# Kernel tuning notes

Measured on AMD Instinct MI355X. Metric: run time of the kernel, lower is better.

The kernel has to match this reference:

```python
import jax, jax.numpy as jnp
import numpy as np

B, T, IN = 65536, 28, 28
H_ENC, H_DEC, N_CLS = 4, 28, 10


def _lstm_params(key, in_dim, hidden):
    k1, k2, k3 = jax.random.split(key, 3)
    s = 1.0 / np.sqrt(hidden)
    Wih = jax.random.uniform(k1, (4 * hidden, in_dim), jnp.float32, -s, s)
    Whh = jax.random.uniform(k2, (4 * hidden, hidden), jnp.float32, -s, s)
    b = jax.random.uniform(k3, (4 * hidden,), jnp.float32, -s, s)  # b_ih + b_hh fused
    return Wih, Whh, b


def setup_inputs() -> dict:
    key = jax.random.key(0)
    kx, ke, kd, ku1, ku2 = jax.random.split(key, 5)
    enc_Wih, enc_Whh, enc_b = _lstm_params(ke, IN, H_ENC)
    dec_Wih, dec_Whh, dec_b = _lstm_params(kd, H_ENC, H_DEC)
    s = 1.0 / np.sqrt(H_DEC)
    U_W = jax.random.uniform(ku1, (N_CLS, H_DEC), jnp.float32, -s, s)
    U_b = jax.random.uniform(ku2, (N_CLS,), jnp.float32, -s, s)
    return {
        "x": jax.random.normal(kx, (B, T, IN), dtype=jnp.float32),
        "enc_Wih": enc_Wih, "enc_Whh": enc_Whh, "enc_b": enc_b,
        "dec_Wih": dec_Wih, "dec_Whh": dec_Whh, "dec_b": dec_b,
        "U_W": U_W, "U_b": U_b,
    }


def _lstm(x, Wih, Whh, b):
    """batch_first LSTM, zero init state. PyTorch gate order i,f,g,o."""
    Bn = x.shape[0]
    H = Whh.shape[1]
    # precompute input projection for all timesteps: [B,T,4H]
    xw = jnp.einsum('bti,gi->btg', x, Wih) + b
    h0 = jnp.zeros((Bn, H), x.dtype)

    def step(carry, xt):
        h, c = carry
        gates = xt + h @ Whh.T
        i, f, g, o = jnp.split(gates, 4, axis=-1)
        c = jax.nn.sigmoid(f) * c + jax.nn.sigmoid(i) * jnp.tanh(g)
        h = jax.nn.sigmoid(o) * jnp.tanh(c)
        return (h, c), h

    (h, c), hs = jax.lax.scan(step, (h0, h0), jnp.swapaxes(xw, 0, 1))
    return jnp.swapaxes(hs, 0, 1), h, c  # [B,T,H], [B,H], [B,H]


def reference(x, enc_Wih, enc_Whh, enc_b, dec_Wih, dec_Whh, dec_b, U_W, U_b):
    x = x.reshape(B, T, IN)
    z, _, _ = _lstm(x, enc_Wih, enc_Whh, enc_b)          # [B,T,4]
    out, h, _ = _lstm(z, dec_Wih, dec_Whh, dec_b)        # [B,T,28], h:[B,28]
    logits = h[None] @ U_W.T + U_b                        # [1,B,10] (h has num_layers=1 leading dim)
    prediction = jax.nn.softmax(logits, axis=2)
    return out, prediction
```

## Files before the change

### kernel.cpp

```cpp
#include <hip/hip_runtime.h>

#define B_TOTAL 65536
#define T_STEPS 28

typedef float f2 __attribute__((ext_vector_type(2)));

__device__ __forceinline__ float frcp(float x) { return __builtin_amdgcn_rcpf(x); }
__device__ __forceinline__ float sigf(float x) { return frcp(1.0f + __expf(-x)); }
__device__ __forceinline__ float tanhf_(float x) { return 2.0f * frcp(1.0f + __expf(-2.0f * x)) - 1.0f; }

__global__ void repack_kernel(const float* __restrict__ eWih, const float* __restrict__ eWhh,
                              const float* __restrict__ eb,
                              const float* __restrict__ dWih, const float* __restrict__ dWhh,
                              const float* __restrict__ db,
                              const float* __restrict__ UW, const float* __restrict__ Ub,
                              float* __restrict__ w)
{
    const int p = threadIdx.x;
    for (int idx = p; idx < 4 * 132; idx += 256) {
        int k = idx / 132, r = idx % 132;
        float v;
        if (r < 4) v = eb[r * 4 + k];
        else {
            int g = (r - 4) / 32, j = (r - 4) % 32;
            v = (j < 28) ? eWih[(g * 4 + k) * 28 + j] : eWhh[(g * 4 + k) * 4 + (j - 28)];
        }
        w[k * 132 + r] = v;
    }
    for (int idx = p; idx < 28 * 132; idx += 256) {
        int k = idx / 132, r = idx % 132;
        float v;
        if (r < 4) v = db[r * 28 + k];
        else {
            int g = (r - 4) / 32, j = (r - 4) % 32;
            v = (j < 28) ? dWhh[(g * 28 + k) * 28 + j] : dWih[(g * 28 + k) * 4 + (j - 28)];
        }
        w[528 + k * 132 + r] = v;
    }
    for (int idx = p; idx < 10 * 32; idx += 256) {
        int c = idx / 32, r = idx % 32;
        float v = (r == 0) ? Ub[c] : ((r <= 28) ? UW[c * 28 + (r - 1)] : 0.f);
        w[4224 + c * 32 + r] = v;
    }
}

#define XB   0
#define HD0  7680
#define HD1  15360
#define HE   23040

__global__ __launch_bounds__(256, 4)
void lstm_main(const float* __restrict__ x, const float* __restrict__ w,
               float* __restrict__ out, float* __restrict__ pred)
{
    __shared__ char lb[25088];

    const int tid  = threadIdx.x;
    const int lane = tid & 63;
    const int s    = __builtin_amdgcn_readfirstlane(tid >> 6);
    const int e0   = blockIdx.x * 64;

    int goff[7], stb[7];
#pragma unroll
    for (int q = 0; q < 7; q++) {
        int idx = tid + 256 * q;
        int i = idx / 28;
        int k = idx - 28 * i;
        goff[q] = i * 784 + k;
        stb[q]  = i * 120 + k * 4;
    }

    const float* __restrict__ xblk = x + (size_t)e0 * 784;
    float* __restrict__ oblk       = out + (size_t)e0 * 784;

#pragma unroll
    for (int q = 0; q < 7; q++)
        *(float*)(lb + XB + stb[q]) = xblk[goff[q]];
    for (int i2 = tid; i2 < 1920; i2 += 256) ((float*)(lb + HD0))[i2] = 0.f;
    ((float*)(lb + HE))[tid] = 0.f;
    __syncthreads();

    const float* __restrict__ wenc = w + s * 132;
    const char* xrow = lb + XB + lane * 120;

    float ce = 0.f;
    float cd[7];
#pragma unroll
    for (int r = 0; r < 7; r++) cd[r] = 0.f;

    int hdc = HD0, hdn = HD1;

    for (int t = 0; t < T_STEPS; ++t) {
        const int p = t & 1;

        float xr[7];
        if (t < T_STEPS - 1) {
#pragma unroll
            for (int q = 0; q < 7; q++)
                xr[q] = xblk[goff[q] + (t + 1) * 28];
        }

        {
            const f2* xp2 = (const f2*)xrow;
            const f2 hep0 = *(const f2*)(lb + HE + p * 1024 + lane * 16);
            const f2 hep1 = *(const f2*)(lb + HE + p * 1024 + lane * 16 + 8);
            const f2* wg0 = (const f2*)(wenc + 4);
            const f2* wg1 = (const f2*)(wenc + 36);
            const f2* wg2 = (const f2*)(wenc + 68);
            const f2* wg3 = (const f2*)(wenc + 100);
            f2 a0 = {wenc[0], 0.f}, a1 = {wenc[1], 0.f};
            f2 a2 = {wenc[2], 0.f}, a3 = {wenc[3], 0.f};
#pragma unroll
            for (int j = 0; j < 14; j++) {
                const f2 v = xp2[j];
                a0 = __builtin_elementwise_fma(wg0[j], v, a0);
                a1 = __builtin_elementwise_fma(wg1[j], v, a1);
                a2 = __builtin_elementwise_fma(wg2[j], v, a2);
                a3 = __builtin_elementwise_fma(wg3[j], v, a3);
            }
            a0 = __builtin_elementwise_fma(wg0[14], hep0, a0);
            a1 = __builtin_elementwise_fma(wg1[14], hep0, a1);
            a2 = __builtin_elementwise_fma(wg2[14], hep0, a2);
            a3 = __builtin_elementwise_fma(wg3[14], hep0, a3);
            a0 = __builtin_elementwise_fma(wg0[15], hep1, a0);
            a1 = __builtin_elementwise_fma(wg1[15], hep1, a1);
            a2 = __builtin_elementwise_fma(wg2[15], hep1, a2);
            a3 = __builtin_elementwise_fma(wg3[15], hep1, a3);
            const float gi = a0.x + a0.y, gf = a1.x + a1.y;
            const float gg = a2.x + a2.y, go = a3.x + a3.y;
            ce = sigf(gf) * ce + sigf(gi) * tanhf_(gg);
            *(float*)(lb + HE + (p ^ 1) * 1024 + lane * 16 + s * 4) =
                sigf(go) * tanhf_(ce);
        }
        __syncthreads();

        {
            const f2 hz0 = *(const f2*)(lb + HE + (p ^ 1) * 1024 + lane * 16);
            const f2 hz1 = *(const f2*)(lb + HE + (p ^ 1) * 1024 + lane * 16 + 8);
            const char* hcr = lb + hdc + lane * 120;
            char* hwr = lb + hdn + lane * 120 + s * 28;
#pragma unroll
            for (int r = 0; r < 7; r++) {
                asm volatile("" ::: "memory");
                const float* __restrict__ wrow = w + 528 + (s * 7 + r) * 132;
                const f2* wg0 = (const f2*)(wrow + 4);
                const f2* wg1 = (const f2*)(wrow + 36);
                const f2* wg2 = (const f2*)(wrow + 68);
                const f2* wg3 = (const f2*)(wrow + 100);
                const f2* hc2 = (const f2*)hcr;
                f2 a0 = {wrow[0], 0.f}, a1 = {wrow[1], 0.f};
                f2 a2 = {wrow[2], 0.f}, a3 = {wrow[3], 0.f};
#pragma unroll
                for (int j = 0; j < 14; j++) {
                    const f2 v = hc2[j];
                    a0 = __builtin_elementwise_fma(wg0[j], v, a0);
                    a1 = __builtin_elementwise_fma(wg1[j], v, a1);
                    a2 = __builtin_elementwise_fma(wg2[j], v, a2);
                    a3 = __builtin_elementwise_fma(wg3[j], v, a3);
                }
                a0 = __builtin_elementwise_fma(wg0[14], hz0, a0);
                a1 = __builtin_elementwise_fma(wg1[14], hz0, a1);
                a2 = __builtin_elementwise_fma(wg2[14], hz0, a2);
                a3 = __builtin_elementwise_fma(wg3[14], hz0, a3);
                a0 = __builtin_elementwise_fma(wg0[15], hz1, a0);
                a1 = __builtin_elementwise_fma(wg1[15], hz1, a1);
                a2 = __builtin_elementwise_fma(wg2[15], hz1, a2);
                a3 = __builtin_elementwise_fma(wg3[15], hz1, a3);
                const float gi = a0.x + a0.y, gf = a1.x + a1.y;
                const float gg = a2.x + a2.y, go = a3.x + a3.y;
                const float cc = sigf(gf) * cd[r] + sigf(gi) * tanhf_(gg);
                cd[r] = cc;
                *(float*)(hwr + r * 4) = sigf(go) * tanhf_(cc);
            }
        }

        if (t < T_STEPS - 1) {
#pragma unroll
            for (int q = 0; q < 7; q++)
                *(float*)(lb + XB + stb[q]) = xr[q];
        }
        __syncthreads();

        {
            const char* hsrc = lb + hdn;
#pragma unroll
            for (int q = 0; q < 7; q++)
                oblk[goff[q] + t * 28] = *(const float*)(hsrc + stb[q]);
        }
        const int tmp = hdc; hdc = hdn; hdn = tmp;
    }

    if (s == 0) {
        float hf[28];
        const f2* hc2 = (const f2*)(lb + hdc + lane * 120);
#pragma unroll
        for (int j = 0; j < 14; j++) {
            const f2 hp = hc2[j];
            hf[2 * j] = hp.x; hf[2 * j + 1] = hp.y;
        }
        float lg[10];
#pragma unroll
        for (int c = 0; c < 10; c++) {
            const float* __restrict__ ur = w + 4224 + c * 32;
            float a = ur[0];
#pragma unroll
            for (int j = 0; j < 28; j++) a = fmaf(ur[1 + j], hf[j], a);
            lg[c] = a;
        }
        float m = lg[0];
#pragma unroll
        for (int c = 1; c < 10; c++) m = fmaxf(m, lg[c]);
        float sum = 0.f;
#pragma unroll
        for (int c = 0; c < 10; c++) { lg[c] = __expf(lg[c] - m); sum += lg[c]; }
        const float inv = frcp(sum);
        float* __restrict__ pr = pred + (size_t)(e0 + lane) * 10;
#pragma unroll
        for (int c = 0; c < 10; c++) pr[c] = lg[c] * inv;
    }
}

extern "C" void kernel_launch(void* const* d_in, const int* in_sizes, int n_in,
                              void* d_out, int out_size, void* d_ws, size_t ws_size,
                              hipStream_t stream) {
    const float* x    = (const float*)d_in[0];
    const float* eWih = (const float*)d_in[1];
    const float* eWhh = (const float*)d_in[2];
    const float* eb   = (const float*)d_in[3];
    const float* dWih = (const float*)d_in[4];
    const float* dWhh = (const float*)d_in[5];
    const float* db   = (const float*)d_in[6];
    const float* UW   = (const float*)d_in[7];
    const float* Ub   = (const float*)d_in[8];

    float* w    = (float*)d_ws;
    float* out  = (float*)d_out;
    float* pred = out + (size_t)B_TOTAL * T_STEPS * 28;

    repack_kernel<<<dim3(1), dim3(256), 0, stream>>>(eWih, eWhh, eb, dWih, dWhh, db, UW, Ub, w);
    lstm_main<<<dim3(B_TOTAL / 64), dim3(256), 0, stream>>>(x, w, out, pred);
}
```

Measured before the change: 542.0 us.

## Software-pipeline encoder one step ahead to halve barriers per timestep

Restructures the time loop so the encoder step for t+1 runs in the same phase as the decoder step for t, with double-buffered x, encoder-h and decoder-h LDS regions. This cuts the block barriers per timestep from two to one, and the barrier becomes a lightweight lgkmcnt wait plus s_barrier. The x prefetch now runs two steps ahead, and output stores are delayed by one step. In exchange LDS grows from about 25KB to 32KB per block, which may limit occupancy.

```diff
diff --git a/kernel.cpp b/kernel.cpp
--- a/kernel.cpp
+++ b/kernel.cpp
@@ -8,6 +8,10 @@
 __device__ __forceinline__ float frcp(float x) { return __builtin_amdgcn_rcpf(x); }
 __device__ __forceinline__ float sigf(float x) { return frcp(1.0f + __expf(-x)); }
 __device__ __forceinline__ float tanhf_(float x) { return 2.0f * frcp(1.0f + __expf(-2.0f * x)) - 1.0f; }
+
+__device__ __forceinline__ void bar_lds() {
+    asm volatile("s_waitcnt lgkmcnt(0)\n\ts_barrier" ::: "memory");
+}
 
 __global__ void repack_kernel(const float* __restrict__ eWih, const float* __restrict__ eWhh,
                               const float* __restrict__ eb,
@@ -44,16 +48,18 @@
     }
 }
 
-#define XB   0
-#define HD0  7680
-#define HD1  15360
-#define HE   23040
+#define XA   0
+#define XB1  7680
+#define HDA  15360
+#define HDB  23040
+#define HEA  30720
+#define HEB  31744
 
 __global__ __launch_bounds__(256, 4)
 void lstm_main(const float* __restrict__ x, const float* __restrict__ w,
                float* __restrict__ out, float* __restrict__ pred)
 {
-    __shared__ char lb[25088];
+    __shared__ char lb[32768];
 
     const int tid  = threadIdx.x;
     const int lane = tid & 63;
@@ -73,72 +79,74 @@
     const float* __restrict__ xblk = x + (size_t)e0 * 784;
     float* __restrict__ oblk       = out + (size_t)e0 * 784;
 
-#pragma unroll
-    for (int q = 0; q < 7; q++)
-        *(float*)(lb + XB + stb[q]) = xblk[goff[q]];
-    for (int i2 = tid; i2 < 1920; i2 += 256) ((float*)(lb + HD0))[i2] = 0.f;
-    ((float*)(lb + HE))[tid] = 0.f;
-    __syncthreads();
-
     const float* __restrict__ wenc = w + s * 132;
-    const char* xrow = lb + XB + lane * 120;
 
     float ce = 0.f;
     float cd[7];
 #pragma unroll
     for (int r = 0; r < 7; r++) cd[r] = 0.f;
 
-    int hdc = HD0, hdn = HD1;
+    auto enc_step = [&](const int xbase, const int hrd, const int hwr) {
+        const f2* xp2 = (const f2*)(lb + xbase + lane * 120);
+        const f2 hep0 = *(const f2*)(lb + hrd + lane * 16);
+        const f2 hep1 = *(const f2*)(lb + hrd + lane * 16 + 8);
+        const f2* wg0 = (const f2*)(wenc + 4);
+        const f2* wg1 = (const f2*)(wenc + 36);
+        const f2* wg2 = (const f2*)(wenc + 68);
+        const f2* wg3 = (const f2*)(wenc + 100);
+        f2 a0 = {wenc[0], 0.f}, a1 = {wenc[1], 0.f};
+        f2 a2 = {wenc[2], 0.f}, a3 = {wenc[3], 0.f};
+#pragma unroll
+        for (int j = 0; j < 14; j++) {
+            const f2 v = xp2[j];
+            a0 = __builtin_elementwise_fma(wg0[j], v, a0);
+            a1 = __builtin_elementwise_fma(wg1[j], v, a1);
+            a2 = __builtin_elementwise_fma(wg2[j], v, a2);
+            a3 = __builtin_elementwise_fma(wg3[j], v, a3);
+        }
+        a0 = __builtin_elementwise_fma(wg0[14], hep0, a0);
+        a1 = __builtin_elementwise_fma(wg1[14], hep0, a1);
+        a2 = __builtin_elementwise_fma(wg2[14], hep0, a2);
+        a3 = __builtin_elementwise_fma(wg3[14], hep0, a3);
+        a0 = __builtin_elementwise_fma(wg0[15], hep1, a0);
+        a1 = __builtin_elementwise_fma(wg1[15], hep1, a1);
+        a2 = __builtin_elementwise_fma(wg2[15], hep1, a2);
+        a3 = __builtin_elementwise_fma(wg3[15], hep1, a3);
+        const float gi = a0.x + a0.y, gf = a1.x + a1.y;
+        const float gg = a2.x + a2.y, go = a3.x + a3.y;
+        ce = sigf(gf) * ce + sigf(gi) * tanhf_(gg);
+        *(float*)(lb + hwr + lane * 16 + s * 4) = sigf(go) * tanhf_(ce);
+    };
+
+#pragma unroll
+    for (int q = 0; q < 7; q++) {
+        *(float*)(lb + XA  + stb[q]) = xblk[goff[q]];
+        *(float*)(lb + XB1 + stb[q]) = xblk[goff[q] + 28];
+    }
+    for (int i2 = tid; i2 < 1920; i2 += 256) ((float*)(lb + HDB))[i2] = 0.f;
+    ((float*)(lb + HEB))[tid] = 0.f;
+    bar_lds();
+
+    enc_step(XA, HEB, HEA);
+    bar_lds();
+
+    int hdc = HDB, hdn = HDA;
+    int her = HEA, hew = HEB;
+    int xe  = XB1, xw  = XA;
 
     for (int t = 0; t < T_STEPS; ++t) {
-        const int p = t & 1;
-
         float xr[7];
-        if (t < T_STEPS - 1) {
+        if (t < T_STEPS - 2) {
 #pragma unroll
             for (int q = 0; q < 7; q++)
-                xr[q] = xblk[goff[q] + (t + 1) * 28];
+                xr[q] = xblk[goff[q] + (t + 2) * 28];
         }
 
         {
-            const f2* xp2 = (const f2*)xrow;
-            const f2 hep0 = *(const f2*)(lb + HE + p * 1024 + lane * 16);
-            const f2 hep1 = *(const f2*)(lb + HE + p * 1024 + lane * 16 + 8);
-            const f2* wg0 = (const f2*)(wenc + 4);
-            const f2* wg1 = (const f2*)(wenc + 36);
-            const f2* wg2 = (const f2*)(wenc + 68);
-            const f2* wg3 = (const f2*)(wenc + 100);
-            f2 a0 = {wenc[0], 0.f}, a1 = {wenc[1], 0.f};
-            f2 a2 = {wenc[2], 0.f}, a3 = {wenc[3], 0.f};
-#pragma unroll
-            for (int j = 0; j < 14; j++) {
-                const f2 v = xp2[j];
-                a0 = __builtin_elementwise_fma(wg0[j], v, a0);
-                a1 = __builtin_elementwise_fma(wg1[j], v, a1);
-                a2 = __builtin_elementwise_fma(wg2[j], v, a2);
-                a3 = __builtin_elementwise_fma(wg3[j], v, a3);
-            }
-            a0 = __builtin_elementwise_fma(wg0[14], hep0, a0);
-            a1 = __builtin_elementwise_fma(wg1[14], hep0, a1);
-            a2 = __builtin_elementwise_fma(wg2[14], hep0, a2);
-            a3 = __builtin_elementwise_fma(wg3[14], hep0, a3);
-            a0 = __builtin_elementwise_fma(wg0[15], hep1, a0);
-            a1 = __builtin_elementwise_fma(wg1[15], hep1, a1);
-            a2 = __builtin_elementwise_fma(wg2[15], hep1, a2);
-            a3 = __builtin_elementwise_fma(wg3[15], hep1, a3);
-            const float gi = a0.x + a0.y, gf = a1.x + a1.y;
-            const float gg = a2.x + a2.y, go = a3.x + a3.y;
-            ce = sigf(gf) * ce + sigf(gi) * tanhf_(gg);
-            *(float*)(lb + HE + (p ^ 1) * 1024 + lane * 16 + s * 4) =
-                sigf(go) * tanhf_(ce);
-        }
-        __syncthreads();
-
-        {
-            const f2 hz0 = *(const f2*)(lb + HE + (p ^ 1) * 1024 + lane * 16);
-            const f2 hz1 = *(const f2*)(lb + HE + (p ^ 1) * 1024 + lane * 16 + 8);
+            const f2 hz0 = *(const f2*)(lb + her + lane * 16);
+            const f2 hz1 = *(const f2*)(lb + her + lane * 16 + 8);
             const char* hcr = lb + hdc + lane * 120;
-            char* hwr = lb + hdn + lane * 120 + s * 28;
+            char* hwrp = lb + hdn + lane * 120 + s * 28;
 #pragma unroll
             for (int r = 0; r < 7; r++) {
                 asm volatile("" ::: "memory");
@@ -170,24 +178,38 @@
                 const float gg = a2.x + a2.y, go = a3.x + a3.y;
                 const float cc = sigf(gf) * cd[r] + sigf(gi) * tanhf_(gg);
                 cd[r] = cc;
-                *(float*)(hwr + r * 4) = sigf(go) * tanhf_(cc);
+                *(float*)(hwrp + r * 4) = sigf(go) * tanhf_(cc);
             }
         }
 
-        if (t < T_STEPS - 1) {
+        if (t < T_STEPS - 1) enc_step(xe, her, hew);
+
+        if (t >= 1) {
+            const char* hsrc = lb + hdc;
 #pragma unroll
             for (int q = 0; q < 7; q++)
-                *(float*)(lb + XB + stb[q]) = xr[q];
-        }
-        __syncthreads();
-
-        {
-            const char* hsrc = lb + hdn;
+                oblk[goff[q] + (t - 1) * 28] = *(const float*)(hsrc + stb[q]);
+        }
+
+        if (t < T_STEPS - 2) {
 #pragma unroll
             for (int q = 0; q < 7; q++)
-                oblk[goff[q] + t * 28] = *(const float*)(hsrc + stb[q]);
-        }
-        const int tmp = hdc; hdc = hdn; hdn = tmp;
+                *(float*)(lb + xw + stb[q]) = xr[q];
+        }
+
+        bar_lds();
+
+        int tmp;
+        tmp = hdc; hdc = hdn; hdn = tmp;
+        tmp = her; her = hew; hew = tmp;
+        tmp = xe;  xe  = xw;  xw  = tmp;
+    }
+
+    {
+        const char* hsrc = lb + hdc;
+#pragma unroll
+        for (int q = 0; q < 7; q++)
+            oblk[goff[q] + 27 * 28] = *(const float*)(hsrc + stb[q]);
     }
 
     if (s == 0) {
```

Measured after the change: 517.7 us. -4.5%, faster.
